# Kernel optimization log

Measured on AMD Instinct MI355X. Metric: run time of the kernel, lower is better.

## Reference

```python
import jax, jax.numpy as jnp
import numpy as np
import math

N_NODES = 100000
N_EDGES = 1600000
IN_F = 64
OUT_F = 64
SUPPORT = 3


def setup_inputs() -> dict:
    key = jax.random.key(0)
    k1, k2, k3, k4, k5, k6 = jax.random.split(key, 6)
    stdv = 1.0 / math.sqrt(OUT_F)
    return {
        "features": jax.random.normal(k1, (N_NODES, IN_F), dtype=jnp.float32),
        "edge_rows": jax.random.randint(k2, (SUPPORT, N_EDGES), 0, N_NODES, dtype=jnp.int32),
        "edge_cols": jax.random.randint(k3, (SUPPORT, N_EDGES), 0, N_NODES, dtype=jnp.int32),
        "edge_vals": jax.random.uniform(k4, (SUPPORT, N_EDGES), dtype=jnp.float32),
        "weight": jax.random.uniform(k5, (IN_F * SUPPORT, OUT_F), minval=-stdv, maxval=stdv, dtype=jnp.float32),
        "bias": jax.random.uniform(k6, (OUT_F,), minval=-stdv, maxval=stdv, dtype=jnp.float32),
    }


def reference(features, edge_rows, edge_cols, edge_vals, weight, bias):
    # Chebyshev GCN layer: out = concat_k(S_k @ X) @ W + b
    n = features.shape[0]

    def spmm(rows, cols, vals):
        # S @ X in COO form: gather source-node features, scale by edge
        # value, scatter-add into destination rows. [E, F] intermediate.
        return jax.ops.segment_sum(vals[:, None] * features[cols], rows, num_segments=n)

    # support is a small fixed constant (3); loop is over supports, not data.
    supports = jnp.concatenate(
        [spmm(edge_rows[k], edge_cols[k], edge_vals[k]) for k in range(edge_rows.shape[0])],
        axis=1,
    )  # [N, support * in_features]
    return supports @ weight + bias
```

## Files before the change

kernel.cpp:

```cpp
#include <hip/hip_runtime.h>


__global__ __launch_bounds__(256) void zero_kernel(int* __restrict__ p, int n) {
  int i = blockIdx.x * 256 + threadIdx.x;
  if (i < n) p[i] = 0;
}

__global__ __launch_bounds__(256) void hist_kernel(
    const int* __restrict__ rows, int* __restrict__ counts,
    int E, int nsup, int N) {
  int i = blockIdx.x * 256 + threadIdx.x;
  if (i < E * nsup) {
    int k = (i >= E) + (i >= 2 * E);
    atomicAdd(&counts[k * N + rows[i]], 1);
  }
}

__global__ __launch_bounds__(512) void scanA_kernel(
    const int* __restrict__ counts, int* __restrict__ blockSums, int M) {
  __shared__ int wsum[8];
  const int t = threadIdx.x;
  const int i0 = blockIdx.x * 2048 + t * 4;
  int s = 0;
  if (i0 + 3 < M) {
    int4 c = *reinterpret_cast<const int4*>(counts + i0);
    s = c.x + c.y + c.z + c.w;
  } else {
#pragma unroll
    for (int u = 0; u < 4; ++u)
      if (i0 + u < M) s += counts[i0 + u];
  }
#pragma unroll
  for (int off = 32; off; off >>= 1) s += __shfl_down(s, off);
  if ((t & 63) == 0) wsum[t >> 6] = s;
  __syncthreads();
  if (t == 0) {
    int tot = 0;
#pragma unroll
    for (int w = 0; w < 8; ++w) tot += wsum[w];
    blockSums[blockIdx.x] = tot;
  }
}

__global__ __launch_bounds__(256) void scanB_kernel(int* __restrict__ bs, int NB) {
  __shared__ int s[2][256];
  int t = threadIdx.x;
  int v = (t < NB) ? bs[t] : 0;
  s[0][t] = v;
  __syncthreads();
  int cur = 0;
  for (int off = 1; off < 256; off <<= 1) {
    int nv = s[cur][t] + ((t >= off) ? s[cur][t - off] : 0);
    s[cur ^ 1][t] = nv;
    cur ^= 1;
    __syncthreads();
  }
  if (t < NB) bs[t] = s[cur][t] - v;
}

__global__ __launch_bounds__(512) void scanC_kernel(
    const int* __restrict__ counts, const int* __restrict__ bs,
    int* __restrict__ offsets, int* __restrict__ cursor, int M) {
  __shared__ int wsum[8];
  const int t = threadIdx.x;
  const int lane = t & 63;
  const int wid = t >> 6;
  const int i0 = blockIdx.x * 2048 + t * 4;
  int c0 = 0, c1 = 0, c2 = 0, c3 = 0;
  if (i0 + 3 < M) {
    int4 c = *reinterpret_cast<const int4*>(counts + i0);
    c0 = c.x; c1 = c.y; c2 = c.z; c3 = c.w;
  } else {
    if (i0 + 0 < M) c0 = counts[i0 + 0];
    if (i0 + 1 < M) c1 = counts[i0 + 1];
    if (i0 + 2 < M) c2 = counts[i0 + 2];
  }
  int s = c0 + c1 + c2 + c3;
  int inc = s;
#pragma unroll
  for (int off = 1; off < 64; off <<= 1) {
    int v = __shfl_up(inc, off);
    if (lane >= off) inc += v;
  }
  if (lane == 63) wsum[wid] = inc;
  __syncthreads();
  int wbase = 0;
#pragma unroll
  for (int w = 0; w < 8; ++w) wbase += (w < wid) ? wsum[w] : 0;
  int excl = bs[blockIdx.x] + wbase + (inc - s);
  int o0 = excl, o1 = o0 + c0, o2 = o1 + c1, o3 = o2 + c2;
  if (i0 + 0 < M) { offsets[i0 + 0] = o0; cursor[i0 + 0] = o0; }
  if (i0 + 1 < M) { offsets[i0 + 1] = o1; cursor[i0 + 1] = o1; }
  if (i0 + 2 < M) { offsets[i0 + 2] = o2; cursor[i0 + 2] = o2; }
  if (i0 + 3 < M) { offsets[i0 + 3] = o3; cursor[i0 + 3] = o3; }
}

__global__ __launch_bounds__(256) void reorder_kernel(
    const int* __restrict__ rows, const int* __restrict__ cols,
    const float* __restrict__ vals, int* __restrict__ cursor,
    int2* __restrict__ packed, int E, int nsup, int N) {
  int i = blockIdx.x * 256 + threadIdx.x;
  if (i < E * nsup) {
    int k = (i >= E) + (i >= 2 * E);
    int r = rows[i];
    int pos = atomicAdd(&cursor[k * N + r], 1);
    packed[pos] = make_int2(cols[i], __float_as_int(vals[i]));
  }
}

__global__ __launch_bounds__(256) void gather_kernel(
    const int2* __restrict__ packed, const int* __restrict__ offs,
    const int* __restrict__ cnts, const float* __restrict__ X,
    const float* __restrict__ Wk, const float* __restrict__ bias,
    float* __restrict__ out, int N, int first) {
  const int lane = threadIdx.x & 63;
  float w[64];
#pragma unroll
  for (int i = 0; i < 64; ++i) w[i] = Wk[i * 64 + lane];
  const int gw0 = (blockIdx.x * 256 + threadIdx.x) >> 6;
  const int nw = (gridDim.x * 256) >> 6;
  for (int r = gw0; r < N; r += nw) {
    const int base = offs[r];
    const int c = cnts[r];
    float acc = 0.f;
    for (int j0 = 0; j0 < c; j0 += 64) {
      int2 p = packed[base + j0 + lane];
      const int lim = min(64, c - j0);
      float a0 = 0.f, a1 = 0.f, a2 = 0.f, a3 = 0.f;
      int j = 0;
      for (; j + 3 < lim; j += 4) {
        int col0 = __builtin_amdgcn_readlane(p.x, j + 0);
        int col1 = __builtin_amdgcn_readlane(p.x, j + 1);
        int col2 = __builtin_amdgcn_readlane(p.x, j + 2);
        int col3 = __builtin_amdgcn_readlane(p.x, j + 3);
        float v0 = __int_as_float(__builtin_amdgcn_readlane(p.y, j + 0));
        float v1 = __int_as_float(__builtin_amdgcn_readlane(p.y, j + 1));
        float v2 = __int_as_float(__builtin_amdgcn_readlane(p.y, j + 2));
        float v3 = __int_as_float(__builtin_amdgcn_readlane(p.y, j + 3));
        float x0 = X[(size_t)col0 * 64 + lane];
        float x1 = X[(size_t)col1 * 64 + lane];
        float x2 = X[(size_t)col2 * 64 + lane];
        float x3 = X[(size_t)col3 * 64 + lane];
        a0 = fmaf(v0, x0, a0);
        a1 = fmaf(v1, x1, a1);
        a2 = fmaf(v2, x2, a2);
        a3 = fmaf(v3, x3, a3);
      }
      for (; j < lim; ++j) {
        int col = __builtin_amdgcn_readlane(p.x, j);
        float v = __int_as_float(__builtin_amdgcn_readlane(p.y, j));
        a0 = fmaf(v, X[(size_t)col * 64 + lane], a0);
      }
      acc += (a0 + a1) + (a2 + a3);
    }
    float o = first ? bias[lane] : out[(size_t)r * 64 + lane];
    const int ai = __float_as_int(acc);
    float p0 = 0.f, p1 = 0.f, p2 = 0.f, p3 = 0.f;
#pragma unroll
    for (int i = 0; i < 16; ++i) {
      p0 = fmaf(__int_as_float(__builtin_amdgcn_readlane(ai, 4 * i + 0)), w[4 * i + 0], p0);
      p1 = fmaf(__int_as_float(__builtin_amdgcn_readlane(ai, 4 * i + 1)), w[4 * i + 1], p1);
      p2 = fmaf(__int_as_float(__builtin_amdgcn_readlane(ai, 4 * i + 2)), w[4 * i + 2], p2);
      p3 = fmaf(__int_as_float(__builtin_amdgcn_readlane(ai, 4 * i + 3)), w[4 * i + 3], p3);
    }
    o += (p0 + p1) + (p2 + p3);
    out[(size_t)r * 64 + lane] = o;
  }
}

extern "C" void kernel_launch(void* const* d_in, const int* in_sizes, int n_in,
                              void* d_out, int out_size, void* d_ws, size_t ws_size,
                              hipStream_t stream) {
  const float* X    = (const float*)d_in[0];
  const int*   rows = (const int*)d_in[1];
  const int*   cols = (const int*)d_in[2];
  const float* vals = (const float*)d_in[3];
  const float* W    = (const float*)d_in[4];
  const float* bias = (const float*)d_in[5];
  float* out = (float*)d_out;

  const int N = in_sizes[0] / 64;
  const int E = in_sizes[1] / 3;

  const size_t padPacked = 64 * sizeof(int2);
  const size_t needFused = (size_t)3 * E * 8 + padPacked + 3 * ((size_t)3 * N * 4) + 2048;
  const bool fused = ws_size >= needFused;
  const int nsup = fused ? 3 : 1;
  const int M = nsup * N;

  char* wp = (char*)d_ws;
  int2* packed   = (int2*)wp;  wp += (size_t)nsup * E * 8 + padPacked;
  int* counts    = (int*)wp;   wp += (size_t)M * 4;
  int* offsets   = (int*)wp;   wp += (size_t)M * 4;
  int* cursor    = (int*)wp;   wp += (size_t)M * 4;
  int* blockSums = (int*)wp;

  const int NB = (M + 2047) / 2048;
  const int zB = (M + 255) / 256;
  const int eB = (E * nsup + 255) / 256;
  const int gatherBlocks = 4096;

  if (fused) {
    zero_kernel<<<zB, 256, 0, stream>>>(counts, M);
    hist_kernel<<<eB, 256, 0, stream>>>(rows, counts, E, 3, N);
    scanA_kernel<<<NB, 512, 0, stream>>>(counts, blockSums, M);
    scanB_kernel<<<1, 256, 0, stream>>>(blockSums, NB);
    scanC_kernel<<<NB, 512, 0, stream>>>(counts, blockSums, offsets, cursor, M);
    reorder_kernel<<<eB, 256, 0, stream>>>(rows, cols, vals, cursor, packed, E, 3, N);
    for (int k = 0; k < 3; ++k)
      gather_kernel<<<gatherBlocks, 256, 0, stream>>>(
          packed, offsets + (size_t)k * N, counts + (size_t)k * N, X,
          W + (size_t)k * 64 * 64, bias, out, N, k == 0 ? 1 : 0);
  } else {
    for (int k = 0; k < 3; ++k) {
      zero_kernel<<<zB, 256, 0, stream>>>(counts, M);
      hist_kernel<<<eB, 256, 0, stream>>>(rows + (size_t)k * E, counts, E, 1, N);
      scanA_kernel<<<NB, 512, 0, stream>>>(counts, blockSums, M);
      scanB_kernel<<<1, 256, 0, stream>>>(blockSums, NB);
      scanC_kernel<<<NB, 512, 0, stream>>>(counts, blockSums, offsets, cursor, M);
      reorder_kernel<<<eB, 256, 0, stream>>>(
          rows + (size_t)k * E, cols + (size_t)k * E, vals + (size_t)k * E,
          cursor, packed, E, 1, N);
      gather_kernel<<<gatherBlocks, 256, 0, stream>>>(
          packed, offsets, counts, X, W + (size_t)k * 64 * 64, bias, out, N,
          k == 0 ? 1 : 0);
    }
  }
}
```

Before: 939.7 us.

## Bin edges by 128-row blocks and accumulate SpMM in shared memory

Replaces the per-row CSR sort with coarse binning of edges into 128-row buckets. Histogram and reorder now use shared-memory atomics per bin, which cuts global atomics. The local row index is packed into the high bits of the column index. A single fused SpMM kernel per bin accumulates all three supports into a 128x64 LDS tile with LDS float atomics, then applies W and bias in registers. The cost is LDS atomic contention, large per-thread register arrays (oacc[32] plus wv[64]), only about 782 blocks, and an assumption that column indices fit in 25 bits.

```diff
diff --git a/kernel.cpp b/kernel.cpp
--- a/kernel.cpp
+++ b/kernel.cpp
@@ -1,18 +1,32 @@
 #include <hip/hip_runtime.h>
 
+
+#define ROWS_PER_BIN 128
+#define MAX_BINS 1024
+#define HIST_EDGES 4096
+#define REORD_EDGES 16384
 
 __global__ __launch_bounds__(256) void zero_kernel(int* __restrict__ p, int n) {
   int i = blockIdx.x * 256 + threadIdx.x;
   if (i < n) p[i] = 0;
 }
 
-__global__ __launch_bounds__(256) void hist_kernel(
-    const int* __restrict__ rows, int* __restrict__ counts,
-    int E, int nsup, int N) {
-  int i = blockIdx.x * 256 + threadIdx.x;
-  if (i < E * nsup) {
-    int k = (i >= E) + (i >= 2 * E);
-    atomicAdd(&counts[k * N + rows[i]], 1);
+__global__ __launch_bounds__(256) void hist_bins_kernel(
+    const int* __restrict__ rows, int* __restrict__ totals,
+    int E, int EB, int NBINS) {
+  __shared__ int lh[MAX_BINS];
+  const int k = blockIdx.x / EB;
+  const int eb = blockIdx.x % EB;
+  for (int b = threadIdx.x; b < NBINS; b += 256) lh[b] = 0;
+  __syncthreads();
+  const int s = eb * HIST_EDGES, e = min(E, s + HIST_EDGES);
+  const size_t kE = (size_t)k * E;
+  for (int i = s + threadIdx.x; i < e; i += 256)
+    atomicAdd(&lh[rows[kE + i] >> 7], 1);
+  __syncthreads();
+  for (int b = threadIdx.x; b < NBINS; b += 256) {
+    int c = lh[b];
+    if (c) atomicAdd(&totals[k * NBINS + b], c);
   }
 }
 
@@ -95,76 +109,119 @@
   if (i0 + 3 < M) { offsets[i0 + 3] = o3; cursor[i0 + 3] = o3; }
 }
 
-__global__ __launch_bounds__(256) void reorder_kernel(
+__global__ __launch_bounds__(256) void reorder_bins_kernel(
     const int* __restrict__ rows, const int* __restrict__ cols,
     const float* __restrict__ vals, int* __restrict__ cursor,
-    int2* __restrict__ packed, int E, int nsup, int N) {
-  int i = blockIdx.x * 256 + threadIdx.x;
-  if (i < E * nsup) {
-    int k = (i >= E) + (i >= 2 * E);
-    int r = rows[i];
-    int pos = atomicAdd(&cursor[k * N + r], 1);
-    packed[pos] = make_int2(cols[i], __float_as_int(vals[i]));
-  }
-}
-
-__global__ __launch_bounds__(256) void gather_kernel(
+    int2* __restrict__ packed, int E, int EB, int NBINS) {
+  __shared__ int lh[MAX_BINS];
+  __shared__ int lbase[MAX_BINS];
+  const int k = blockIdx.x / EB;
+  const int eb = blockIdx.x % EB;
+  for (int b = threadIdx.x; b < NBINS; b += 256) lh[b] = 0;
+  __syncthreads();
+  const int s = eb * REORD_EDGES, e = min(E, s + REORD_EDGES);
+  const size_t kE = (size_t)k * E;
+  for (int i = s + threadIdx.x; i < e; i += 256)
+    atomicAdd(&lh[rows[kE + i] >> 7], 1);
+  __syncthreads();
+  for (int b = threadIdx.x; b < NBINS; b += 256) {
+    int c = lh[b];
+    lbase[b] = c ? atomicAdd(&cursor[k * NBINS + b], c) : 0;
+  }
+  __syncthreads();
+  for (int b = threadIdx.x; b < NBINS; b += 256) lh[b] = 0;
+  __syncthreads();
+  for (int i = s + threadIdx.x; i < e; i += 256) {
+    int r = rows[kE + i];
+    int bin = r >> 7, lr = r & 127;
+    int lp = atomicAdd(&lh[bin], 1);
+    packed[lbase[bin] + lp] =
+        make_int2(cols[kE + i] | (lr << 25), __float_as_int(vals[kE + i]));
+  }
+}
+
+__global__ __launch_bounds__(256) void spmm_bins_kernel(
     const int2* __restrict__ packed, const int* __restrict__ offs,
-    const int* __restrict__ cnts, const float* __restrict__ X,
-    const float* __restrict__ Wk, const float* __restrict__ bias,
-    float* __restrict__ out, int N, int first) {
+    const float* __restrict__ X, const float* __restrict__ W,
+    const float* __restrict__ bias, float* __restrict__ out,
+    int N, int NBINS, int kFirst, int kCount, int totalE) {
+  __shared__ float acc[ROWS_PER_BIN * 64];
+  const int bin = blockIdx.x;
   const int lane = threadIdx.x & 63;
-  float w[64];
-#pragma unroll
-  for (int i = 0; i < 64; ++i) w[i] = Wk[i * 64 + lane];
-  const int gw0 = (blockIdx.x * 256 + threadIdx.x) >> 6;
-  const int nw = (gridDim.x * 256) >> 6;
-  for (int r = gw0; r < N; r += nw) {
-    const int base = offs[r];
-    const int c = cnts[r];
-    float acc = 0.f;
-    for (int j0 = 0; j0 < c; j0 += 64) {
-      int2 p = packed[base + j0 + lane];
-      const int lim = min(64, c - j0);
-      float a0 = 0.f, a1 = 0.f, a2 = 0.f, a3 = 0.f;
+  const int wid = threadIdx.x >> 6;
+  float oacc[32];
+#pragma unroll
+  for (int i = 0; i < 32; ++i) oacc[i] = 0.f;
+
+  for (int kl = 0; kl < kCount; ++kl) {
+    for (int idx = threadIdx.x; idx < ROWS_PER_BIN * 64; idx += 256)
+      acc[idx] = 0.f;
+    __syncthreads();
+    const int segIdx = kl * NBINS + bin;
+    const int s = offs[segIdx];
+    const int e = (segIdx + 1 < kCount * NBINS) ? offs[segIdx + 1] : totalE;
+    for (int b2 = s + wid * 64; b2 < e; b2 += 256) {
+      int2 p = packed[b2 + lane];
+      const int lim = min(64, e - b2);
       int j = 0;
       for (; j + 3 < lim; j += 4) {
-        int col0 = __builtin_amdgcn_readlane(p.x, j + 0);
-        int col1 = __builtin_amdgcn_readlane(p.x, j + 1);
-        int col2 = __builtin_amdgcn_readlane(p.x, j + 2);
-        int col3 = __builtin_amdgcn_readlane(p.x, j + 3);
+        unsigned q0 = (unsigned)__builtin_amdgcn_readlane(p.x, j + 0);
+        unsigned q1 = (unsigned)__builtin_amdgcn_readlane(p.x, j + 1);
+        unsigned q2 = (unsigned)__builtin_amdgcn_readlane(p.x, j + 2);
+        unsigned q3 = (unsigned)__builtin_amdgcn_readlane(p.x, j + 3);
         float v0 = __int_as_float(__builtin_amdgcn_readlane(p.y, j + 0));
         float v1 = __int_as_float(__builtin_amdgcn_readlane(p.y, j + 1));
         float v2 = __int_as_float(__builtin_amdgcn_readlane(p.y, j + 2));
         float v3 = __int_as_float(__builtin_amdgcn_readlane(p.y, j + 3));
-        float x0 = X[(size_t)col0 * 64 + lane];
-        float x1 = X[(size_t)col1 * 64 + lane];
-        float x2 = X[(size_t)col2 * 64 + lane];
-        float x3 = X[(size_t)col3 * 64 + lane];
-        a0 = fmaf(v0, x0, a0);
-        a1 = fmaf(v1, x1, a1);
-        a2 = fmaf(v2, x2, a2);
-        a3 = fmaf(v3, x3, a3);
+        float x0 = X[(size_t)(q0 & 0x1FFFFFFu) * 64 + lane];
+        float x1 = X[(size_t)(q1 & 0x1FFFFFFu) * 64 + lane];
+        float x2 = X[(size_t)(q2 & 0x1FFFFFFu) * 64 + lane];
+        float x3 = X[(size_t)(q3 & 0x1FFFFFFu) * 64 + lane];
+        atomicAdd(&acc[(q0 >> 25) * 64 + lane], v0 * x0);
+        atomicAdd(&acc[(q1 >> 25) * 64 + lane], v1 * x1);
+        atomicAdd(&acc[(q2 >> 25) * 64 + lane], v2 * x2);
+        atomicAdd(&acc[(q3 >> 25) * 64 + lane], v3 * x3);
       }
       for (; j < lim; ++j) {
-        int col = __builtin_amdgcn_readlane(p.x, j);
+        unsigned q = (unsigned)__builtin_amdgcn_readlane(p.x, j);
         float v = __int_as_float(__builtin_amdgcn_readlane(p.y, j));
-        a0 = fmaf(v, X[(size_t)col * 64 + lane], a0);
+        float x = X[(size_t)(q & 0x1FFFFFFu) * 64 + lane];
+        atomicAdd(&acc[(q >> 25) * 64 + lane], v * x);
       }
-      acc += (a0 + a1) + (a2 + a3);
-    }
-    float o = first ? bias[lane] : out[(size_t)r * 64 + lane];
-    const int ai = __float_as_int(acc);
-    float p0 = 0.f, p1 = 0.f, p2 = 0.f, p3 = 0.f;
-#pragma unroll
-    for (int i = 0; i < 16; ++i) {
-      p0 = fmaf(__int_as_float(__builtin_amdgcn_readlane(ai, 4 * i + 0)), w[4 * i + 0], p0);
-      p1 = fmaf(__int_as_float(__builtin_amdgcn_readlane(ai, 4 * i + 1)), w[4 * i + 1], p1);
-      p2 = fmaf(__int_as_float(__builtin_amdgcn_readlane(ai, 4 * i + 2)), w[4 * i + 2], p2);
-      p3 = fmaf(__int_as_float(__builtin_amdgcn_readlane(ai, 4 * i + 3)), w[4 * i + 3], p3);
-    }
-    o += (p0 + p1) + (p2 + p3);
-    out[(size_t)r * 64 + lane] = o;
+    }
+    __syncthreads();
+    const int kk = kFirst + kl;
+    float wv[64];
+#pragma unroll
+    for (int i = 0; i < 64; ++i) wv[i] = W[((size_t)kk * 64 + i) * 64 + lane];
+#pragma unroll
+    for (int i = 0; i < 32; ++i) {
+      const int lr = wid * 32 + i;
+      const int row = bin * ROWS_PER_BIN + lr;
+      if (row < N) {
+        int ai = __float_as_int(acc[lr * 64 + lane]);
+        float p0 = 0.f, p1 = 0.f, p2 = 0.f, p3 = 0.f;
+#pragma unroll
+        for (int m = 0; m < 16; ++m) {
+          p0 = fmaf(__int_as_float(__builtin_amdgcn_readlane(ai, 4 * m + 0)), wv[4 * m + 0], p0);
+          p1 = fmaf(__int_as_float(__builtin_amdgcn_readlane(ai, 4 * m + 1)), wv[4 * m + 1], p1);
+          p2 = fmaf(__int_as_float(__builtin_amdgcn_readlane(ai, 4 * m + 2)), wv[4 * m + 2], p2);
+          p3 = fmaf(__int_as_float(__builtin_amdgcn_readlane(ai, 4 * m + 3)), wv[4 * m + 3], p3);
+        }
+        oacc[i] += (p0 + p1) + (p2 + p3);
+      }
+    }
+    __syncthreads();
+  }
+#pragma unroll
+  for (int i = 0; i < 32; ++i) {
+    const int lr = wid * 32 + i;
+    const int row = bin * ROWS_PER_BIN + lr;
+    if (row < N) {
+      float v = oacc[i];
+      v += (kFirst == 0) ? bias[lane] : out[(size_t)row * 64 + lane];
+      out[(size_t)row * 64 + lane] = v;
+    }
   }
 }
 
@@ -181,49 +238,49 @@
 
   const int N = in_sizes[0] / 64;
   const int E = in_sizes[1] / 3;
-
-  const size_t padPacked = 64 * sizeof(int2);
-  const size_t needFused = (size_t)3 * E * 8 + padPacked + 3 * ((size_t)3 * N * 4) + 2048;
+  const int NBINS = (N + ROWS_PER_BIN - 1) / ROWS_PER_BIN;
+  const int EBh = (E + HIST_EDGES - 1) / HIST_EDGES;
+  const int EBr = (E + REORD_EDGES - 1) / REORD_EDGES;
+
+  const size_t needFused =
+      ((size_t)3 * E + 64) * 8 + 3 * ((size_t)3 * NBINS * 4) + 2048;
   const bool fused = ws_size >= needFused;
   const int nsup = fused ? 3 : 1;
-  const int M = nsup * N;
+  const int M = nsup * NBINS;
 
   char* wp = (char*)d_ws;
-  int2* packed   = (int2*)wp;  wp += (size_t)nsup * E * 8 + padPacked;
-  int* counts    = (int*)wp;   wp += (size_t)M * 4;
-  int* offsets   = (int*)wp;   wp += (size_t)M * 4;
+  int2* packed   = (int2*)wp;  wp += ((size_t)nsup * E + 64) * 8;
+  int* totals    = (int*)wp;   wp += (size_t)M * 4;
+  int* offs      = (int*)wp;   wp += (size_t)M * 4;
   int* cursor    = (int*)wp;   wp += (size_t)M * 4;
   int* blockSums = (int*)wp;
 
   const int NB = (M + 2047) / 2048;
   const int zB = (M + 255) / 256;
-  const int eB = (E * nsup + 255) / 256;
-  const int gatherBlocks = 4096;
 
   if (fused) {
-    zero_kernel<<<zB, 256, 0, stream>>>(counts, M);
-    hist_kernel<<<eB, 256, 0, stream>>>(rows, counts, E, 3, N);
-    scanA_kernel<<<NB, 512, 0, stream>>>(counts, blockSums, M);
+    zero_kernel<<<zB, 256, 0, stream>>>(totals, M);
+    hist_bins_kernel<<<3 * EBh, 256, 0, stream>>>(rows, totals, E, EBh, NBINS);
+    scanA_kernel<<<NB, 512, 0, stream>>>(totals, blockSums, M);
     scanB_kernel<<<1, 256, 0, stream>>>(blockSums, NB);
-    scanC_kernel<<<NB, 512, 0, stream>>>(counts, blockSums, offsets, cursor, M);
-    reorder_kernel<<<eB, 256, 0, stream>>>(rows, cols, vals, cursor, packed, E, 3, N);
-    for (int k = 0; k < 3; ++k)
-      gather_kernel<<<gatherBlocks, 256, 0, stream>>>(
-          packed, offsets + (size_t)k * N, counts + (size_t)k * N, X,
-          W + (size_t)k * 64 * 64, bias, out, N, k == 0 ? 1 : 0);
+    scanC_kernel<<<NB, 512, 0, stream>>>(totals, blockSums, offs, cursor, M);
+    reorder_bins_kernel<<<3 * EBr, 256, 0, stream>>>(
+        rows, cols, vals, cursor, packed, E, EBr, NBINS);
+    spmm_bins_kernel<<<NBINS, 256, 0, stream>>>(
+        packed, offs, X, W, bias, out, N, NBINS, 0, 3, 3 * E);
   } else {
     for (int k = 0; k < 3; ++k) {
-      zero_kernel<<<zB, 256, 0, stream>>>(counts, M);
-      hist_kernel<<<eB, 256, 0, stream>>>(rows + (size_t)k * E, counts, E, 1, N);
-      scanA_kernel<<<NB, 512, 0, stream>>>(counts, blockSums, M);
+      zero_kernel<<<zB, 256, 0, stream>>>(totals, M);
+      hist_bins_kernel<<<EBh, 256, 0, stream>>>(
+          rows + (size_t)k * E, totals, E, EBh, NBINS);
+      scanA_kernel<<<NB, 512, 0, stream>>>(totals, blockSums, M);
       scanB_kernel<<<1, 256, 0, stream>>>(blockSums, NB);
-      scanC_kernel<<<NB, 512, 0, stream>>>(counts, blockSums, offsets, cursor, M);
-      reorder_kernel<<<eB, 256, 0, stream>>>(
+      scanC_kernel<<<NB, 512, 0, stream>>>(totals, blockSums, offs, cursor, M);
+      reorder_bins_kernel<<<EBr, 256, 0, stream>>>(
           rows + (size_t)k * E, cols + (size_t)k * E, vals + (size_t)k * E,
-          cursor, packed, E, 1, N);
-      gather_kernel<<<gatherBlocks, 256, 0, stream>>>(
-          packed, offsets, counts, X, W + (size_t)k * 64 * 64, bias, out, N,
-          k == 0 ? 1 : 0);
-    }
-  }
-}
+          cursor, packed, E, EBr, NBINS);
+      spmm_bins_kernel<<<NBINS, 256, 0, stream>>>(
+          packed, offs, X, W, bias, out, N, NBINS, k, 1, E);
+    }
+  }
+}
```

After: 2.305 ms. 2.45x slower.
